# Kernel tuning notes

Hardware: AMD Instinct MI355X
Metric: run time of the kernel (lower is better)

## Reference

```python
import jax, jax.numpy as jnp
import numpy as np

H = 16            # num heads
D = 64            # head dim
HID = 1024        # hidden size
ALPHA = 1.0       # < 2 -> power-law kernel
BANDWIDTH = 1.0
A = 0.5           # doubly-stochastic exponent
RADIUS = 1.0      # sphere radius
EPS = 1e-7


def setup_inputs() -> dict:
    key = jax.random.key(0)
    ks = jax.random.split(key, 5)
    x = jax.random.normal(ks[0], (2, 2048, HID), dtype=jnp.float32)
    s = 1.0 / np.sqrt(HID)
    qkv_w = jax.random.normal(ks[1], (3 * HID, HID), dtype=jnp.float32) * s
    qkv_b = jnp.zeros((3 * HID,), dtype=jnp.float32)
    out_w = jax.random.normal(ks[2], (HID, HID), dtype=jnp.float32) * s
    out_b = jnp.zeros((HID,), dtype=jnp.float32)
    return {"x": x, "qkv_w": qkv_w, "qkv_b": qkv_b, "out_w": out_w, "out_b": out_b}


def _l2norm(t):
    # torch F.normalize(p=2, dim=-1): divide by max(||t||, 1e-12)
    n = jnp.sqrt(jnp.sum(t * t, axis=-1, keepdims=True))
    return t / jnp.maximum(n, 1e-12)


def reference(x, qkv_w, qkv_b, out_w, out_b):
    B, S, _ = x.shape
    qkv = x @ qkv_w.T + qkv_b                       # [B,S,3*HID]
    q, k, v = jnp.split(qkv, 3, axis=-1)
    # [B,H,S,D]
    q = _l2norm(q.reshape(B, S, H, D).transpose(0, 2, 1, 3))
    k = _l2norm(k.reshape(B, S, H, D).transpose(0, 2, 1, 3))
    v = v.reshape(B, S, H, D).transpose(0, 2, 1, 3)
    # geodesic distance on the sphere
    cos = jnp.clip(jnp.einsum('bhsd,bhtd->bhst', q, k), -1.0 + EPS, 1.0 - EPS)
    g_dist = jnp.arccos(cos) * RADIUS               # [B,H,S,S]
    # alpha < 2: power-law kernel
    attn_score = (1.0 + g_dist / jnp.sqrt(BANDWIDTH)) ** (-(D + ALPHA))
    # doubly-stochastic-style rescale: diag(row^-a) @ K @ diag(col^-a)
    row = attn_score.sum(-1) ** (-A)                # [B,H,S]
    col = attn_score.sum(-2) ** (-A)                # [B,H,S]
    k_tilde = row[..., :, None] * attn_score * col[..., None, :]
    # F.normalize(p=1, dim=3): divide by max(sum |.|, 1e-12); entries >= 0
    probs = k_tilde / jnp.maximum(k_tilde.sum(-1, keepdims=True), 1e-12)
    out = jnp.einsum('bhst,bhtd->bhsd', probs, v)   # [B,H,S,D]
    out = out.transpose(0, 2, 1, 3).reshape(B, S, HID)
    return out @ out_w.T + out_b
```

## Files before the change

### kernel.cpp

```cpp
#include <hip/hip_runtime.h>
#include <math.h>

#define NH   16
#define HD   64
#define HIDN 1024
#define NB   2
#define SEQ  2048
#define ROWS (NB*SEQ)
#define BH   (NB*NH)

typedef __attribute__((ext_vector_type(8))) short bf16x8;
typedef __attribute__((ext_vector_type(8))) _Float16 f16x8;
typedef __attribute__((ext_vector_type(4))) float f32x4;
typedef _Float16 f16;

__device__ __forceinline__ unsigned short f2bf(float f) {
    unsigned u = __float_as_uint(f);
    u += 0x7FFF + ((u >> 16) & 1);
    return (unsigned short)(u >> 16);
}
__device__ __forceinline__ bf16x8 ldfrag(const unsigned short* p) {
    return *(const bf16x8*)p;
}
__device__ __forceinline__ f16x8 ldfragh(const f16* p) {
    return *(const f16x8*)p;
}
__device__ __forceinline__ f32x4 mfma16(bf16x8 a, bf16x8 b, f32x4 c) {
    return __builtin_amdgcn_mfma_f32_16x16x32_bf16(a, b, c, 0, 0, 0);
}
__device__ __forceinline__ f32x4 mfma16h(f16x8 a, f16x8 b, f32x4 c) {
    return __builtin_amdgcn_mfma_f32_16x16x32_f16(a, b, c, 0, 0, 0);
}

__device__ __forceinline__ float score_fast(float c) {
    float u = 1.0f - c;
    u = fminf(fmaxf(u, 1e-7f), 2.0f - 1e-7f);
    float s = __builtin_amdgcn_sqrtf(2.0f * u);
    float p = fmaf(u, 6.9907e-4f, 1.8988e-3f);
    p = fmaf(u, p, 5.5804e-3f);
    p = fmaf(u, p, 1.8750e-2f);
    p = fmaf(u, p, 8.3333336e-2f);
    p = fmaf(u, p, 1.0f);
    float g = s * p;
    float l = __builtin_amdgcn_logf(1.0f + g);
    return __builtin_amdgcn_exp2f(-65.0f * l);
}

__global__ __launch_bounds__(256)
void conv_f16(const float* __restrict__ src, f16* __restrict__ dst) {
    int i = (blockIdx.x * 256 + threadIdx.x) * 8;
    float4 a = *(const float4*)(src + i);
    float4 b = *(const float4*)(src + i + 4);
    f16x8 o = { (f16)a.x, (f16)a.y, (f16)a.z, (f16)a.w,
                (f16)b.x, (f16)b.y, (f16)b.z, (f16)b.w };
    *(f16x8*)(dst + i) = o;
}

__global__ __launch_bounds__(256)
void gemm_nt_f16(const f16* __restrict__ A, const f16* __restrict__ B,
                 const float* __restrict__ bias, float* __restrict__ C,
                 int M, int N, int K)
{
    __shared__ f16 As[128 * 32];
    __shared__ f16 Bs[128 * 32];
    const int tid = threadIdx.x;
    const int lane = tid & 63, w = tid >> 6;
    const int ln = lane & 15, lq = lane >> 4;
    const int wm = (w >> 1) * 64, wn = (w & 1) * 64;
    const int m0 = blockIdx.x * 128, n0 = blockIdx.y * 128;

    const int srow = tid >> 1;
    const int scol = (tid & 1) * 16;
    const f16* Ag = A + (size_t)(m0 + srow) * K + scol;
    const f16* Bg = B + (size_t)(n0 + srow) * K + scol;
    f16* Asw = As + srow * 32 + scol;
    f16* Bsw = Bs + srow * 32 + scol;

    f32x4 acc[4][4];
    #pragma unroll
    for (int i = 0; i < 4; ++i)
        #pragma unroll
        for (int j = 0; j < 4; ++j) acc[i][j] = (f32x4){0.f, 0.f, 0.f, 0.f};

    for (int kc = 0; kc < K; kc += 32) {
        uint4 a0 = *(const uint4*)(Ag + kc);
        uint4 a1 = *(const uint4*)(Ag + kc + 8);
        uint4 b0 = *(const uint4*)(Bg + kc);
        uint4 b1 = *(const uint4*)(Bg + kc + 8);
        __syncthreads();
        *(uint4*)Asw = a0; *(uint4*)(Asw + 8) = a1;
        *(uint4*)Bsw = b0; *(uint4*)(Bsw + 8) = b1;
        __syncthreads();
        f16x8 af[4], bf[4];
        #pragma unroll
        for (int i = 0; i < 4; ++i)
            af[i] = *(const f16x8*)&As[(wm + i * 16 + ln) * 32 + lq * 8];
        #pragma unroll
        for (int j = 0; j < 4; ++j)
            bf[j] = *(const f16x8*)&Bs[(wn + j * 16 + ln) * 32 + lq * 8];
        #pragma unroll
        for (int i = 0; i < 4; ++i)
            #pragma unroll
            for (int j = 0; j < 4; ++j)
                acc[i][j] = mfma16h(af[i], bf[j], acc[i][j]);
    }

    #pragma unroll
    for (int i = 0; i < 4; ++i) {
        #pragma unroll
        for (int j = 0; j < 4; ++j) {
            int colIdx = n0 + wn + j * 16 + ln;
            float bs = bias[colIdx];
            #pragma unroll
            for (int r = 0; r < 4; ++r) {
                int row = m0 + wm + i * 16 + lq * 4 + r;
                C[(size_t)row * N + colIdx] = acc[i][j][r] + bs;
            }
        }
    }
}

__global__ __launch_bounds__(256)
void normalize_qk_f16(const float* __restrict__ qkv,
                      f16* __restrict__ qf, f16* __restrict__ kf)
{
    int w    = blockIdx.x * 4 + (threadIdx.x >> 6);
    int lane = threadIdx.x & 63;
    int n = w >> 4, h = w & 15;
    int b = n >> 11, s = n & 2047;
    const float* base = qkv + (size_t)n * 3 * HIDN + h * HD;
    float q = base[lane], k = base[HIDN + lane];
    float qs = q * q, ks = k * k;
    #pragma unroll
    for (int o = 32; o; o >>= 1) { qs += __shfl_xor(qs, o); ks += __shfl_xor(ks, o); }
    q *= 1.0f / fmaxf(sqrtf(qs), 1e-12f);
    k *= 1.0f / fmaxf(sqrtf(ks), 1e-12f);
    size_t idx = ((size_t)((b * NH + h) * SEQ + s)) * HD + lane;
    qf[idx] = (f16)q;
    kf[idx] = (f16)k;
}

__global__ __launch_bounds__(256)
void v_transpose(const float* __restrict__ qkv, unsigned short* __restrict__ vth)
{
    __shared__ float Ls[64][65];
    int bh = blockIdx.y, s0 = blockIdx.x * 64;
    int b = bh >> 4, h = bh & 15;
    int tid = threadIdx.x;
    #pragma unroll
    for (int i = 0; i < 4; ++i) {
        int idx = tid + i * 256;
        int row = idx >> 4, c4 = (idx & 15) * 4;
        float4 v = *(const float4*)&qkv[((size_t)(b * SEQ + s0 + row)) * 3 * HIDN
                                        + 2 * HIDN + h * HD + c4];
        Ls[row][c4+0] = v.x; Ls[row][c4+1] = v.y; Ls[row][c4+2] = v.z; Ls[row][c4+3] = v.w;
    }
    __syncthreads();
    int d = tid >> 2, sb = (tid & 3) * 16;
    unsigned short hi[16];
    #pragma unroll
    for (int j = 0; j < 16; ++j) hi[j] = f2bf(Ls[sb + j][d]);
    size_t o = ((size_t)bh * HD + d) * SEQ + s0 + sb;
    *(uint4*)&vth[o]     = *(uint4*)&hi[0];
    *(uint4*)&vth[o + 8] = *(uint4*)&hi[8];
}

#define KSTR 72

__global__ __launch_bounds__(256)
void col_sum_f16(const f16* __restrict__ qf, const f16* __restrict__ kf,
                 float* __restrict__ colp)
{
    __shared__ __align__(16) f16 Qs[64 * KSTR];
    int bh = blockIdx.y, z = blockIdx.z;
    int tid = threadIdx.x, w = tid >> 6, lane = tid & 63, ln = lane & 15, lq = lane >> 4;
    int m0 = blockIdx.x * 64 + w * 16;
    int s_base = z * (SEQ / 2);
    const f16* qb = qf + (size_t)bh * SEQ * HD;
    const int sr = tid >> 3;
    const int sc = (tid & 7) * 8;

    size_t rowK = ((size_t)bh * SEQ + m0 + ln) * HD;
    f16x8 kf0 = ldfragh(kf + rowK + lq * 8), kf1 = ldfragh(kf + rowK + 32 + lq * 8);

    uint4 qa = *(const uint4*)(qb + (size_t)(s_base + sr) * HD + sc);
    uint4 qc = *(const uint4*)(qb + (size_t)(s_base + sr + 32) * HD + sc);

    float cacc[4] = {0.f, 0.f, 0.f, 0.f};
    #pragma unroll 1
    for (int st = 0; st < SEQ / 128; ++st) {
        __syncthreads();
        *(uint4*)&Qs[sr * KSTR + sc] = qa;
        *(uint4*)&Qs[(sr + 32) * KSTR + sc] = qc;
        int sn = s_base + ((st + 1 < SEQ / 128) ? (st + 1) * 64 : 0);
        qa = *(const uint4*)(qb + (size_t)(sn + sr) * HD + sc);
        qc = *(const uint4*)(qb + (size_t)(sn + sr + 32) * HD + sc);
        __syncthreads();
        #pragma unroll
        for (int nt = 0; nt < 4; ++nt) {
            const f16* qp = &Qs[(nt * 16 + ln) * KSTR + lq * 8];
            f32x4 sacc = {0.f, 0.f, 0.f, 0.f};
            sacc = mfma16h(kf0, *(const f16x8*)qp, sacc);
            sacc = mfma16h(kf1, *(const f16x8*)(qp + 32), sacc);
            #pragma unroll
            for (int r = 0; r < 4; ++r) cacc[r] += score_fast(sacc[r]);
        }
    }
    #pragma unroll
    for (int r = 0; r < 4; ++r) {
        float v = cacc[r];
        v += __shfl_xor(v, 1); v += __shfl_xor(v, 2);
        v += __shfl_xor(v, 4); v += __shfl_xor(v, 8);
        if (ln == 0)
            colp[((size_t)z * BH + bh) * SEQ + m0 + lq * 4 + r] = v;
    }
}

__global__ __launch_bounds__(256)
void col_finalize(const float* __restrict__ colp, float* __restrict__ col)
{
    int i = (blockIdx.x * 256 + threadIdx.x) * 4;
    float4 a = *(const float4*)&colp[i];
    float4 b = *(const float4*)&colp[(size_t)BH * SEQ + i];
    float4 o;
    o.x = 1.0f / sqrtf(a.x + b.x);
    o.y = 1.0f / sqrtf(a.y + b.y);
    o.z = 1.0f / sqrtf(a.z + b.z);
    o.w = 1.0f / sqrtf(a.w + b.w);
    *(float4*)&col[i] = o;
}

__global__ __launch_bounds__(256)
void attn_f16(const f16* __restrict__ qf, const f16* __restrict__ kf,
              const unsigned short* __restrict__ vth,
              const float* __restrict__ col,
              float* __restrict__ nump, float* __restrict__ denp)
{
    __shared__ __align__(16) f16 Ks[64 * KSTR];
    __shared__ __align__(16) unsigned short Vs[64 * KSTR];
    __shared__ __align__(16) unsigned short Ws[4][16 * KSTR];
    __shared__ float cls[64];
    int bh = blockIdx.y, z = blockIdx.z;
    int tid = threadIdx.x, w = tid >> 6, lane = tid & 63, ln = lane & 15, lq = lane >> 4;
    int m0 = blockIdx.x * 64 + w * 16;
    int t_base = z * (SEQ / 2);
    unsigned short* ws = Ws[w];

    const f16* kb = kf + (size_t)bh * SEQ * HD;
    const unsigned short* vb = vth + (size_t)bh * HD * SEQ;
    const float* cb = col + (size_t)bh * SEQ;

    const int sr = tid >> 3;
    const int sc = (tid & 7) * 8;

    size_t rowQ = ((size_t)bh * SEQ + m0 + ln) * HD;
    f16x8 qf0 = ldfragh(qf + rowQ + lq * 8), qf1 = ldfragh(qf + rowQ + 32 + lq * 8);

    f32x4 num[4];
    #pragma unroll
    for (int nt = 0; nt < 4; ++nt) num[nt] = (f32x4){0.f, 0.f, 0.f, 0.f};
    float dpart[4] = {0.f, 0.f, 0.f, 0.f};

    uint4 ka = *(const uint4*)(kb + (size_t)(t_base + sr) * HD + sc);
    uint4 kc = *(const uint4*)(kb + (size_t)(t_base + sr + 32) * HD + sc);
    uint4 va = *(const uint4*)(vb + (size_t)sr * SEQ + t_base + sc);
    uint4 vc = *(const uint4*)(vb + (size_t)(sr + 32) * SEQ + t_base + sc);
    float clv = (tid < 64) ? cb[t_base + tid] : 0.f;

    #pragma unroll 1
    for (int tt = 0; tt < SEQ / 128; ++tt) {
        __syncthreads();
        *(uint4*)&Ks[sr * KSTR + sc] = ka;
        *(uint4*)&Ks[(sr + 32) * KSTR + sc] = kc;
        *(uint4*)&Vs[sr * KSTR + sc] = va;
        *(uint4*)&Vs[(sr + 32) * KSTR + sc] = vc;
        if (tid < 64) cls[tid] = clv;
        int tn = t_base + ((tt + 1 < SEQ / 128) ? (tt + 1) * 64 : 0);
        ka = *(const uint4*)(kb + (size_t)(tn + sr) * HD + sc);
        kc = *(const uint4*)(kb + (size_t)(tn + sr + 32) * HD + sc);
        va = *(const uint4*)(vb + (size_t)sr * SEQ + tn + sc);
        vc = *(const uint4*)(vb + (size_t)(sr + 32) * SEQ + tn + sc);
        clv = (tid < 64) ? cb[tn + tid] : 0.f;
        __syncthreads();

        #pragma unroll
        for (int nt = 0; nt < 4; ++nt) {
            const f16* kp = &Ks[(nt * 16 + ln) * KSTR + lq * 8];
            f32x4 sacc = {0.f, 0.f, 0.f, 0.f};
            sacc = mfma16h(qf0, *(const f16x8*)kp, sacc);
            sacc = mfma16h(qf1, *(const f16x8*)(kp + 32), sacc);
            float cl = cls[nt * 16 + ln];
            #pragma unroll
            for (int r = 0; r < 4; ++r) {
                float wv = score_fast(sacc[r]) * cl;
                dpart[r] += wv;
                ws[(lq * 4 + r) * KSTR + nt * 16 + ln] = f2bf(wv);
            }
        }
        bf16x8 wa0 = ldfrag(ws + ln * KSTR + lq * 8);
        bf16x8 wa1 = ldfrag(ws + ln * KSTR + 32 + lq * 8);
        #pragma unroll
        for (int nt = 0; nt < 4; ++nt) {
            const unsigned short* vp = &Vs[(nt * 16 + ln) * KSTR + lq * 8];
            num[nt] = mfma16(wa0, *(const bf16x8*)vp, num[nt]);
            num[nt] = mfma16(wa1, *(const bf16x8*)(vp + 32), num[nt]);
        }
    }

    #pragma unroll
    for (int r = 0; r < 4; ++r) {
        float v = dpart[r];
        v += __shfl_xor(v, 1); v += __shfl_xor(v, 2);
        v += __shfl_xor(v, 4); v += __shfl_xor(v, 8);
        if (ln == 0)
            denp[((size_t)z * BH + bh) * SEQ + m0 + lq * 4 + r] = v;
    }
    float* np = nump + (((size_t)z * BH + bh) * (SEQ / 64) + blockIdx.x) * 4096
                + (size_t)(w * 16) * 64;
    #pragma unroll
    for (int nt = 0; nt < 4; ++nt)
        #pragma unroll
        for (int r = 0; r < 4; ++r)
            np[(lq * 4 + r) * 64 + nt * 16 + ln] = num[nt][r];
}

__global__ __launch_bounds__(256)
void attn_combine(const float* __restrict__ nump, const float* __restrict__ denp,
                  f16* __restrict__ ctx)
{
    int sT = blockIdx.x, bh = blockIdx.y;
    int b = bh >> 4, h = bh & 15;
    int tid = threadIdx.x;
    int s_l = tid >> 2, dg = (tid & 3) * 16;
    const float* p0 = nump + (((size_t)bh) * (SEQ / 64) + sT) * 4096 + s_l * 64 + dg;
    const float* p1 = nump + (((size_t)BH + bh) * (SEQ / 64) + sT) * 4096 + s_l * 64 + dg;
    int s = sT * 64 + s_l;
    float den = denp[(size_t)bh * SEQ + s] + denp[((size_t)BH + bh) * SEQ + s];
    float inv = 1.0f / fmaxf(den, 1e-12f);
    f16 o[16];
    #pragma unroll
    for (int j4 = 0; j4 < 4; ++j4) {
        float4 a = *(const float4*)(p0 + j4 * 4);
        float4 c = *(const float4*)(p1 + j4 * 4);
        o[j4*4+0] = (f16)((a.x + c.x) * inv);
        o[j4*4+1] = (f16)((a.y + c.y) * inv);
        o[j4*4+2] = (f16)((a.z + c.z) * inv);
        o[j4*4+3] = (f16)((a.w + c.w) * inv);
    }
    f16* dst = ctx + ((size_t)(b * SEQ + s)) * HIDN + h * HD + dg;
    *(f16x8*)dst = *(f16x8*)&o[0];
    *(f16x8*)(dst + 8) = *(f16x8*)&o[8];
}

extern "C" void kernel_launch(void* const* d_in, const int* in_sizes, int n_in,
                              void* d_out, int out_size, void* d_ws, size_t ws_size,
                              hipStream_t stream) {
    const float* x      = (const float*)d_in[0];
    const float* qkv_w  = (const float*)d_in[1];
    const float* qkv_b  = (const float*)d_in[2];
    const float* out_w  = (const float*)d_in[3];
    const float* out_b  = (const float*)d_in[4];
    float* out = (float*)d_out;

    const size_t NTT = (size_t)BH * SEQ * HD;
    float* qkv = (float*)d_ws;
    float* nump = qkv;
    float* denp = nump + (size_t)2 * BH * (SEQ/64) * 4096;
    float* colp = denp + (size_t)2 * BH * SEQ;
    float* col = qkv + (size_t)ROWS * 3 * HIDN;
    f16* xh    = (f16*)(col + (size_t)BH * SEQ);
    f16* wqh   = xh + (size_t)ROWS * HIDN;
    f16* woh   = wqh + (size_t)3 * HIDN * HIDN;
    f16* ctxh  = woh + (size_t)HIDN * HIDN;
    f16* qfp   = ctxh + (size_t)ROWS * HIDN;
    f16* kfp   = qfp + NTT;
    unsigned short* vth = (unsigned short*)(kfp + NTT);

    conv_f16<<<ROWS*HIDN/2048, 256, 0, stream>>>(x, xh);
    conv_f16<<<3*HIDN*HIDN/2048, 256, 0, stream>>>(qkv_w, wqh);
    conv_f16<<<HIDN*HIDN/2048, 256, 0, stream>>>(out_w, woh);

    gemm_nt_f16<<<dim3(ROWS/128, 3*HIDN/128), 256, 0, stream>>>(
        xh, wqh, qkv_b, qkv, ROWS, 3*HIDN, HIDN);
    normalize_qk_f16<<<ROWS*NH/4, 256, 0, stream>>>(qkv, qfp, kfp);
    v_transpose<<<dim3(SEQ/64, BH), 256, 0, stream>>>(qkv, vth);
    col_sum_f16<<<dim3(SEQ/64, BH, 2), 256, 0, stream>>>(qfp, kfp, colp);
    col_finalize<<<BH*SEQ/1024, 256, 0, stream>>>(colp, col);
    attn_f16<<<dim3(SEQ/64, BH, 2), 256, 0, stream>>>(qfp, kfp, vth, col, nump, denp);
    attn_combine<<<dim3(SEQ/64, BH), 256, 0, stream>>>(nump, denp, ctxh);
    gemm_nt_f16<<<dim3(ROWS/128, HIDN/128), 256, 0, stream>>>(
        ctxh, woh, out_b, out, ROWS, HIDN, HIDN);
}
```

Before: 360.4 us.

## Fold column scale into log domain, compute denominator via MFMA, shrink LDS stride

Rewrites the score function as a shorter polynomial that returns log2(1+acos) directly, and stores col as a log-scale so the multiply by the column factor becomes an add inside the exp2. The row denominator is now accumulated with an MFMA against a ones vector instead of scalar adds and shuffles, and bf16 conversion is replaced by truncation. The LDS row stride drops from 72 to 68. These cut VALU work in the attention inner loop, at the cost of slightly lower precision from truncation and the denominator now summing bf16-rounded weights. The new stride may also cause LDS bank conflicts or misalign the 16-byte fragment loads.

```diff
diff --git a/kernel.cpp b/kernel.cpp
--- a/kernel.cpp
+++ b/kernel.cpp
@@ -32,18 +32,14 @@
     return __builtin_amdgcn_mfma_f32_16x16x32_f16(a, b, c, 0, 0, 0);
 }
 
-__device__ __forceinline__ float score_fast(float c) {
-    float u = 1.0f - c;
-    u = fminf(fmaxf(u, 1e-7f), 2.0f - 1e-7f);
-    float s = __builtin_amdgcn_sqrtf(2.0f * u);
-    float p = fmaf(u, 6.9907e-4f, 1.8988e-3f);
-    p = fmaf(u, p, 5.5804e-3f);
-    p = fmaf(u, p, 1.8750e-2f);
-    p = fmaf(u, p, 8.3333336e-2f);
-    p = fmaf(u, p, 1.0f);
-    float g = s * p;
-    float l = __builtin_amdgcn_logf(1.0f + g);
-    return __builtin_amdgcn_exp2f(-65.0f * l);
+__device__ __forceinline__ float log2_1pacos(float c) {
+    float u = fmaxf(1.0f - c, 0.0f);
+    float s = __builtin_amdgcn_sqrtf(u);
+    float p = fmaf(u, 2.68532e-3f, 7.89259e-3f);
+    p = fmaf(u, p, 2.6516504e-2f);
+    p = fmaf(u, p, 1.1785113e-1f);
+    p = fmaf(u, p, 1.4142136f);
+    return __builtin_amdgcn_logf(fmaf(s, p, 1.0f));
 }
 
 __global__ __launch_bounds__(256)
@@ -165,7 +161,7 @@
     *(uint4*)&vth[o + 8] = *(uint4*)&hi[8];
 }
 
-#define KSTR 72
+#define KSTR 68
 
 __global__ __launch_bounds__(256)
 void col_sum_f16(const f16* __restrict__ qf, const f16* __restrict__ kf,
@@ -203,7 +199,8 @@
             sacc = mfma16h(kf0, *(const f16x8*)qp, sacc);
             sacc = mfma16h(kf1, *(const f16x8*)(qp + 32), sacc);
             #pragma unroll
-            for (int r = 0; r < 4; ++r) cacc[r] += score_fast(sacc[r]);
+            for (int r = 0; r < 4; ++r)
+                cacc[r] += __builtin_amdgcn_exp2f(-65.0f * log2_1pacos(sacc[r]));
         }
     }
     #pragma unroll
@@ -223,10 +220,10 @@
     float4 a = *(const float4*)&colp[i];
     float4 b = *(const float4*)&colp[(size_t)BH * SEQ + i];
     float4 o;
-    o.x = 1.0f / sqrtf(a.x + b.x);
-    o.y = 1.0f / sqrtf(a.y + b.y);
-    o.z = 1.0f / sqrtf(a.z + b.z);
-    o.w = 1.0f / sqrtf(a.w + b.w);
+    o.x = -0.5f * __builtin_amdgcn_logf(a.x + b.x);
+    o.y = -0.5f * __builtin_amdgcn_logf(a.y + b.y);
+    o.z = -0.5f * __builtin_amdgcn_logf(a.z + b.z);
+    o.w = -0.5f * __builtin_amdgcn_logf(a.w + b.w);
     *(float4*)&col[i] = o;
 }
 
@@ -239,7 +236,7 @@
     __shared__ __align__(16) f16 Ks[64 * KSTR];
     __shared__ __align__(16) unsigned short Vs[64 * KSTR];
     __shared__ __align__(16) unsigned short Ws[4][16 * KSTR];
-    __shared__ float cls[64];
+    __shared__ float lcls[64];
     int bh = blockIdx.y, z = blockIdx.z;
     int tid = threadIdx.x, w = tid >> 6, lane = tid & 63, ln = lane & 15, lq = lane >> 4;
     int m0 = blockIdx.x * 64 + w * 16;
@@ -256,10 +253,14 @@
     size_t rowQ = ((size_t)bh * SEQ + m0 + ln) * HD;
     f16x8 qf0 = ldfragh(qf + rowQ + lq * 8), qf1 = ldfragh(qf + rowQ + 32 + lq * 8);
 
+    bf16x8 ones;
+    #pragma unroll
+    for (int i = 0; i < 8; ++i) ones[i] = (short)0x3F80;
+
     f32x4 num[4];
     #pragma unroll
     for (int nt = 0; nt < 4; ++nt) num[nt] = (f32x4){0.f, 0.f, 0.f, 0.f};
-    float dpart[4] = {0.f, 0.f, 0.f, 0.f};
+    f32x4 den = {0.f, 0.f, 0.f, 0.f};
 
     uint4 ka = *(const uint4*)(kb + (size_t)(t_base + sr) * HD + sc);
     uint4 kc = *(const uint4*)(kb + (size_t)(t_base + sr + 32) * HD + sc);
@@ -274,7 +275,7 @@
         *(uint4*)&Ks[(sr + 32) * KSTR + sc] = kc;
         *(uint4*)&Vs[sr * KSTR + sc] = va;
         *(uint4*)&Vs[(sr + 32) * KSTR + sc] = vc;
-        if (tid < 64) cls[tid] = clv;
+        if (tid < 64) lcls[tid] = clv;
         int tn = t_base + ((tt + 1 < SEQ / 128) ? (tt + 1) * 64 : 0);
         ka = *(const uint4*)(kb + (size_t)(tn + sr) * HD + sc);
         kc = *(const uint4*)(kb + (size_t)(tn + sr + 32) * HD + sc);
@@ -289,16 +290,19 @@
             f32x4 sacc = {0.f, 0.f, 0.f, 0.f};
             sacc = mfma16h(qf0, *(const f16x8*)kp, sacc);
             sacc = mfma16h(qf1, *(const f16x8*)(kp + 32), sacc);
-            float cl = cls[nt * 16 + ln];
+            float lcl = lcls[nt * 16 + ln];
             #pragma unroll
             for (int r = 0; r < 4; ++r) {
-                float wv = score_fast(sacc[r]) * cl;
-                dpart[r] += wv;
-                ws[(lq * 4 + r) * KSTR + nt * 16 + ln] = f2bf(wv);
+                float l = log2_1pacos(sacc[r]);
+                float wv = __builtin_amdgcn_exp2f(fmaf(l, -65.0f, lcl));
+                ws[(lq * 4 + r) * KSTR + nt * 16 + ln] =
+                    (unsigned short)(__float_as_uint(wv) >> 16);
             }
         }
         bf16x8 wa0 = ldfrag(ws + ln * KSTR + lq * 8);
         bf16x8 wa1 = ldfrag(ws + ln * KSTR + 32 + lq * 8);
+        den = mfma16(wa0, ones, den);
+        den = mfma16(wa1, ones, den);
         #pragma unroll
         for (int nt = 0; nt < 4; ++nt) {
             const unsigned short* vp = &Vs[(nt * 16 + ln) * KSTR + lq * 8];
@@ -307,13 +311,10 @@
         }
     }
 
-    #pragma unroll
-    for (int r = 0; r < 4; ++r) {
-        float v = dpart[r];
-        v += __shfl_xor(v, 1); v += __shfl_xor(v, 2);
-        v += __shfl_xor(v, 4); v += __shfl_xor(v, 8);
-        if (ln == 0)
-            denp[((size_t)z * BH + bh) * SEQ + m0 + lq * 4 + r] = v;
+    if (ln == 0) {
+        #pragma unroll
+        for (int r = 0; r < 4; ++r)
+            denp[((size_t)z * BH + bh) * SEQ + m0 + lq * 4 + r] = den[r];
     }
     float* np = nump + (((size_t)z * BH + bh) * (SEQ / 64) + blockIdx.x) * 4096
                 + (size_t)(w * 16) * 64;
```

Result: slower. 578.2 us (+60.4%).
